# Optimization experiments

Measured on AMD Instinct MI355X. Metric: run time of the kernel, lower is better.

The kernel has to match this reference:

```python
import jax, jax.numpy as jnp
import numpy as np

B, N1, N2, D = 4096, 16, 32, 30   # node batch, 1st-hop nbrs, 2nd-hop nbrs, nodeDataLen
H, HD = 6, 5                       # heads, head_dim (embed_dim = size_out*heads = 30)
LH = 64                            # linear_hidden
NEG_SLOPE = 0.02


def setup_inputs() -> dict:
    key = jax.random.key(0)
    ks = jax.random.split(key, 20)
    def w(k, shape, std=0.2):
        return jax.random.normal(k, shape, dtype=jnp.float32) * std
    return {
        "x2": jax.random.normal(ks[0], (B, N1, N2, D), dtype=jnp.float32),
        "self_feat": jax.random.normal(ks[1], (B, D), dtype=jnp.float32),
        # second-hop GraphLayer params (size_in=30 -> embed 30)
        "lin_w2": w(ks[2], (D, D)), "lin_b2": jnp.zeros((D,), jnp.float32),
        "in_w2": w(ks[3], (3 * D, D), 0.1), "in_b2": jnp.zeros((3 * D,), jnp.float32),
        "out_w2": w(ks[4], (D, D), 0.1), "out_b2": jnp.zeros((D,), jnp.float32),
        # first-hop GraphLayer params
        "lin_w1": w(ks[5], (D, D)), "lin_b1": jnp.zeros((D,), jnp.float32),
        "in_w1": w(ks[6], (3 * D, D), 0.1), "in_b1": jnp.zeros((3 * D,), jnp.float32),
        "out_w1": w(ks[7], (D, D), 0.1), "out_b1": jnp.zeros((D,), jnp.float32),
        # classification MLP
        "cw1": w(ks[8], (LH, D), 0.02), "cb1": jnp.zeros((LH,), jnp.float32),
        "cw2": w(ks[9], (LH, LH), 0.02), "cb2": jnp.zeros((LH,), jnp.float32),
        "cw3": w(ks[10], (2, LH), 0.02), "cb3": jnp.zeros((2,), jnp.float32),
    }


def graph_layer(x, lw, lb, iw, ib, ow, ob):
    """x: [S, D] -> Linear + LeakyReLU(0.02) + MHA(self) + mean over S -> [D].
    Dropout(0.2) is identity in eval mode."""
    S = x.shape[0]
    y = jax.nn.leaky_relu(x @ lw.T + lb, NEG_SLOPE)          # [S, D]
    qkv = y @ iw.T + ib                                       # [S, 3D] packed in_proj
    q, k, v = jnp.split(qkv, 3, axis=-1)
    q = q.reshape(S, H, HD)
    k = k.reshape(S, H, HD)
    v = v.reshape(S, H, HD)
    scores = jnp.einsum('shd,thd->hst', q, k) / np.float32(np.sqrt(HD))
    att = jax.nn.softmax(scores, axis=-1)                     # [H, S, S]
    o = jnp.einsum('hst,thd->shd', att, v).reshape(S, H * HD) # [S, D]
    o = o @ ow.T + ob
    return o.mean(axis=0)                                     # [D]


def reference(x2, self_feat,
              lin_w2, lin_b2, in_w2, in_b2, out_w2, out_b2,
              lin_w1, lin_b1, in_w1, in_b1, out_w1, out_b1,
              cw1, cb1, cw2, cb2, cw3, cb3):
    gl2 = lambda x: graph_layer(x, lin_w2, lin_b2, in_w2, in_b2, out_w2, out_b2)
    h1 = jax.vmap(jax.vmap(gl2))(x2)                          # [B, N1, D] second-hop aggregation
    seq = jnp.concatenate([h1, self_feat[:, None, :]], axis=1)  # [B, N1+1, D] append current node
    gl1 = lambda x: graph_layer(x, lin_w1, lin_b1, in_w1, in_b1, out_w1, out_b1)
    emb = jax.vmap(gl1)(seq)                                  # [B, D]
    h = jax.nn.leaky_relu(emb @ cw1.T + cb1, NEG_SLOPE)
    h = jax.nn.leaky_relu(h @ cw2.T + cb2, NEG_SLOPE)
    logits = h @ cw3.T + cb3                                  # [B, 2]
    # original applies Softmax(dim=0) to the 1-D 2-vector per node == softmax over classes
    return jax.nn.softmax(logits, axis=-1)
```

## Files before the change

kernel.cpp:

```cpp
#include <hip/hip_runtime.h>
#include <math.h>

#define LRELU(v) fmaxf((v), 0.02f * (v))

typedef __attribute__((ext_vector_type(8)))  short short8;
typedef __attribute__((ext_vector_type(4)))  float f32x4;
typedef __attribute__((ext_vector_type(16))) float f32x16;
typedef __attribute__((ext_vector_type(2)))  int   int2v;
typedef __attribute__((ext_vector_type(4)))  int   int4v;

__device__ inline short f2bf(float f) {
    unsigned u = __builtin_bit_cast(unsigned, f);
    unsigned r = (u + 0x7FFFu + ((u >> 16) & 1u)) >> 16;
    return (short)r;
}
__device__ inline int cvt_pk_bf16(float lo, float hi) {
    int r;
    asm("v_cvt_pk_bf16_f32 %0, %1, %2" : "=v"(r) : "v"(lo), "v"(hi));
    return r;
}
__device__ inline float exp2_asm(float x) {
    float r;
    asm("v_exp_f32 %0, %1" : "=v"(r) : "v"(x));
    return r;
}

#define RS5L  0.6451994329f

__global__ __launch_bounds__(256, 4) void fused_kernel(
    const float* __restrict__ x2, const float* __restrict__ self_feat,
    const float* __restrict__ lw2, const float* __restrict__ lb2,
    const float* __restrict__ iw2, const float* __restrict__ ib2,
    const float* __restrict__ ow2, const float* __restrict__ ob2,
    const float* __restrict__ lw1, const float* __restrict__ lb1,
    const float* __restrict__ iw1, const float* __restrict__ ib1,
    const float* __restrict__ ow1, const float* __restrict__ ob1,
    const float* __restrict__ cw1, const float* __restrict__ cb1,
    const float* __restrict__ cw2, const float* __restrict__ cb2,
    const float* __restrict__ cw3, const float* __restrict__ cb3,
    float* __restrict__ out)
{
    __shared__ __attribute__((aligned(16))) short y_lds[2][32][40];
    __shared__ __attribute__((aligned(16))) short qmf[2][6][33][8];
    __shared__ __attribute__((aligned(16))) short kmf[2][6][33][8];
    __shared__ __attribute__((aligned(16))) short vbf[2][6][8][40];
    __shared__ __attribute__((aligned(16))) float h1f[16][33];
    __shared__ float obar[2][32];
    __shared__ float embb[32];
    __shared__ float hb1[64];
    __shared__ float hb2[64];
    __shared__ float lg[2];

    const int tid  = threadIdx.x;
    const int lane = tid & 63;
    const int w    = tid >> 6;
    const int l15  = lane & 15;
    const int lq   = lane >> 4;
    const int h5   = lane >> 5;
    const int scol = lane & 31;
    const int rowz = (lane < 32) ? scol : 32;

    for (int i = tid; i < 1584; i += 256) { ((int*)qmf)[i] = 0; ((int*)kmf)[i] = 0; }
    for (int i = tid; i < 1920; i += 256) ((int*)vbf)[i] = 0;
    if (tid < 4) obar[tid >> 1][30 + (tid & 1)] = 0.0f;

    const int di = w & 1, si = w >> 1;
    const int jtA = (3 * w) >> 1, jtB = (3 * w + 2) >> 1;
    short8 blw2f; float lbv2v;
    {
        int d = di * 16 + l15;
        #pragma unroll
        for (int i = 0; i < 8; ++i) {
            int k = lq * 8 + i;
            blw2f[i] = f2bf((d < 30 && k < 30) ? lw2[d * 30 + k] : 0.0f);
        }
        lbv2v = (d < 30) ? lb2[d] : 0.0f;
    }
    short8 biwA2, biwB2; float ibvA2, ibvB2;
    {
        int jA = jtA * 16 + l15, jB = jtB * 16 + l15;
        #pragma unroll
        for (int i = 0; i < 8; ++i) {
            int k = lq * 8 + i;
            biwA2[i] = f2bf((jA < 90 && k < 30) ? iw2[jA * 30 + k] : 0.0f);
            biwB2[i] = f2bf((jB < 90 && k < 30) ? iw2[jB * 30 + k] : 0.0f);
        }
        ibvA2 = (jA < 90) ? ib2[jA] : 0.0f;
        ibvB2 = (jB < 90) ? ib2[jB] : 0.0f;
    }
    __syncthreads();

    const long node = (long)blockIdx.x;
    const float* xbase = x2 + node * (16L * 960);
    const float* sfp   = self_feat + node * 30;

    for (int it = 0; it < 8; ++it) {

        {
            int s = si * 16 + l15;
            #pragma unroll
            for (int pr = 0; pr < 2; ++pr) {
                const float* xr = xbase + (2 * it + pr) * 960 + s * 30 + lq * 8;
                float xv[8];
                #pragma unroll
                for (int i = 0; i < 8; ++i) {
                    int k = lq * 8 + i;
                    xv[i] = (k < 30) ? xr[i] : 0.0f;
                }
                int4v ai;
                ai.x = cvt_pk_bf16(xv[0], xv[1]);
                ai.y = cvt_pk_bf16(xv[2], xv[3]);
                ai.z = cvt_pk_bf16(xv[4], xv[5]);
                ai.w = cvt_pk_bf16(xv[6], xv[7]);
                short8 af = __builtin_bit_cast(short8, ai);
                f32x4 c = {0.0f, 0.0f, 0.0f, 0.0f};
                c = __builtin_amdgcn_mfma_f32_16x16x32_bf16(af, blw2f, c, 0, 0, 0);
                float y0 = LRELU(c[0] + lbv2v), y1 = LRELU(c[1] + lbv2v);
                float y2 = LRELU(c[2] + lbv2v), y3 = LRELU(c[3] + lbv2v);
                int p01 = cvt_pk_bf16(y0, y1), p23 = cvt_pk_bf16(y2, y3);
                int row = si * 16 + lq * 4, col = di * 16 + l15;
                y_lds[pr][row + 0][col] = (short)p01;
                y_lds[pr][row + 1][col] = (short)(p01 >> 16);
                y_lds[pr][row + 2][col] = (short)p23;
                y_lds[pr][row + 3][col] = (short)(p23 >> 16);
            }
        }
        __syncthreads();

        {
            #pragma unroll
            for (int pr = 0; pr < 2; ++pr) {
                short8 a0 = *(const short8*)&y_lds[pr][l15][lq * 8];
                short8 a1 = *(const short8*)&y_lds[pr][16 + l15][lq * 8];
                #pragma unroll
                for (int t = 0; t < 3; ++t) {
                    int T = 3 * w + t, jt = T >> 1, si_ = T & 1;
                    short8 a = si_ ? a1 : a0;
                    short8 b = (jt == jtA) ? biwA2 : biwB2;
                    float ibv = (jt == jtA) ? ibvA2 : ibvB2;
                    f32x4 c = {0.0f, 0.0f, 0.0f, 0.0f};
                    c = __builtin_amdgcn_mfma_f32_16x16x32_bf16(a, b, c, 0, 0, 0);
                    int j = jt * 16 + l15;
                    int s0 = si_ * 16 + lq * 4;
                    if (j < 30) {
                        int h = j / 5, e = j - 5 * h;
                        int p01 = cvt_pk_bf16(c[0] + ibv, c[1] + ibv);
                        int p23 = cvt_pk_bf16(c[2] + ibv, c[3] + ibv);
                        qmf[pr][h][s0 + 0][e] = (short)p01;
                        qmf[pr][h][s0 + 1][e] = (short)(p01 >> 16);
                        qmf[pr][h][s0 + 2][e] = (short)p23;
                        qmf[pr][h][s0 + 3][e] = (short)(p23 >> 16);
                    } else if (j < 60) {
                        int jj = j - 30; int h = jj / 5, e = jj - 5 * h;
                        float ibl = ibv * RS5L;
                        int p01 = cvt_pk_bf16(fmaf(c[0], RS5L, ibl), fmaf(c[1], RS5L, ibl));
                        int p23 = cvt_pk_bf16(fmaf(c[2], RS5L, ibl), fmaf(c[3], RS5L, ibl));
                        kmf[pr][h][s0 + 0][e] = (short)p01;
                        kmf[pr][h][s0 + 1][e] = (short)(p01 >> 16);
                        kmf[pr][h][s0 + 2][e] = (short)p23;
                        kmf[pr][h][s0 + 3][e] = (short)(p23 >> 16);
                    } else if (j < 90) {
                        int jj = j - 60; int h = jj / 5, e = jj - 5 * h;
                        int k0 = ((s0 >> 1) & 4) | ((s0 << 1) & 8) | (s0 & 16);
                        int2v wv;
                        wv.x = cvt_pk_bf16(c[0] + ibv, c[1] + ibv);
                        wv.y = cvt_pk_bf16(c[2] + ibv, c[3] + ibv);
                        *(int2v*)&vbf[pr][h][e][k0] = wv;
                    }
                }
            }
        }
        __syncthreads();

        {
            const int pr = w >> 1;
            #pragma unroll
            for (int hh = 0; hh < 3; ++hh) {
                const int h = 3 * (w & 1) + hh;
                short8 af = *(const short8*)&kmf[pr][h][rowz][0];
                short8 bf = *(const short8*)&qmf[pr][h][rowz][0];
                f32x16 c;
                #pragma unroll
                for (int r = 0; r < 16; ++r) c[r] = 0.0f;
                c = __builtin_amdgcn_mfma_f32_32x32x16_bf16(af, bf, c, 0, 0, 0);
                float m = c[0];
                #pragma unroll
                for (int r = 1; r < 16; ++r) m = fmaxf(m, c[r]);
                m = fmaxf(m, __shfl_xor(m, 32));
                float Z = 0.0f;
                #pragma unroll
                for (int r = 0; r < 16; ++r) { c[r] = exp2_asm(c[r] - m); Z += c[r]; }
                Z += __shfl_xor(Z, 32);
                float rZ = __builtin_amdgcn_rcpf(Z) * (1.0f / 32.0f);
                int4v a1i, a2i;
                a1i.x = cvt_pk_bf16(c[0] * rZ,  c[1] * rZ);
                a1i.y = cvt_pk_bf16(c[2] * rZ,  c[3] * rZ);
                a1i.z = cvt_pk_bf16(c[4] * rZ,  c[5] * rZ);
                a1i.w = cvt_pk_bf16(c[6] * rZ,  c[7] * rZ);
                a2i.x = cvt_pk_bf16(c[8] * rZ,  c[9] * rZ);
                a2i.y = cvt_pk_bf16(c[10] * rZ, c[11] * rZ);
                a2i.z = cvt_pk_bf16(c[12] * rZ, c[13] * rZ);
                a2i.w = cvt_pk_bf16(c[14] * rZ, c[15] * rZ);
                short8 b1 = *(const short8*)&vbf[pr][h][scol & 7][8 * h5];
                short8 b2 = *(const short8*)&vbf[pr][h][scol & 7][16 + 8 * h5];
                f32x16 P;
                #pragma unroll
                for (int r = 0; r < 16; ++r) P[r] = 0.0f;
                P = __builtin_amdgcn_mfma_f32_32x32x16_bf16(
                        __builtin_bit_cast(short8, a1i), b1, P, 0, 0, 0);
                P = __builtin_amdgcn_mfma_f32_32x32x16_bf16(
                        __builtin_bit_cast(short8, a2i), b2, P, 0, 0, 0);
                float sm = 0.0f;
                #pragma unroll
                for (int r = 0; r < 16; ++r) sm += P[r];
                sm += __shfl_xor(sm, 32);
                if (lane < 5) obar[pr][h * 5 + lane] = sm;
            }
        }
        __syncthreads();

        if (tid < 240) {
            const int d = tid >> 3, jq = tid & 7;
            #pragma unroll
            for (int pr = 0; pr < 2; ++pr) {
                f32x4 ov = *(const f32x4*)&obar[pr][jq * 4];
                float part = 0.0f;
                #pragma unroll
                for (int i = 0; i < 4; ++i) {
                    int j = jq * 4 + i;
                    if (j < 30) part = fmaf(ov[i], ow2[d * 30 + j], part);
                }
                part += __shfl_down(part, 4, 8);
                part += __shfl_down(part, 2, 8);
                part += __shfl_down(part, 1, 8);
                if (jq == 0) h1f[2 * it + pr][d] = part + ob2[d];
            }
        }
    }
    __syncthreads();

    short8 blw1f; float lbv1v;
    {
        int d = di * 16 + l15;
        #pragma unroll
        for (int i = 0; i < 8; ++i) {
            int k = lq * 8 + i;
            blw1f[i] = f2bf((d < 30 && k < 30) ? lw1[d * 30 + k] : 0.0f);
        }
        lbv1v = (d < 30) ? lb1[d] : 0.0f;
    }
    short8 biwA1, biwB1; float ibvA1, ibvB1;
    {
        int jA = jtA * 16 + l15, jB = jtB * 16 + l15;
        #pragma unroll
        for (int i = 0; i < 8; ++i) {
            int k = lq * 8 + i;
            biwA1[i] = f2bf((jA < 90 && k < 30) ? iw1[jA * 30 + k] : 0.0f);
            biwB1[i] = f2bf((jB < 90 && k < 30) ? iw1[jB * 30 + k] : 0.0f);
        }
        ibvA1 = (jA < 90) ? ib1[jA] : 0.0f;
        ibvB1 = (jB < 90) ? ib1[jB] : 0.0f;
    }

    {
        float xv[8];
        if (si == 0) {
            #pragma unroll
            for (int i = 0; i < 8; ++i) {
                int k = lq * 8 + i;
                xv[i] = (k < 30) ? h1f[l15][k] : 0.0f;
            }
        } else {
            #pragma unroll
            for (int i = 0; i < 8; ++i) {
                int k = lq * 8 + i;
                xv[i] = (l15 == 0 && k < 30) ? sfp[k] : 0.0f;
            }
        }
        int4v ai;
        ai.x = cvt_pk_bf16(xv[0], xv[1]);
        ai.y = cvt_pk_bf16(xv[2], xv[3]);
        ai.z = cvt_pk_bf16(xv[4], xv[5]);
        ai.w = cvt_pk_bf16(xv[6], xv[7]);
        short8 af = __builtin_bit_cast(short8, ai);
        f32x4 c = {0.0f, 0.0f, 0.0f, 0.0f};
        c = __builtin_amdgcn_mfma_f32_16x16x32_bf16(af, blw1f, c, 0, 0, 0);
        float y0 = LRELU(c[0] + lbv1v), y1 = LRELU(c[1] + lbv1v);
        float y2 = LRELU(c[2] + lbv1v), y3 = LRELU(c[3] + lbv1v);
        int p01 = cvt_pk_bf16(y0, y1), p23 = cvt_pk_bf16(y2, y3);
        int row = si * 16 + lq * 4, col = di * 16 + l15;
        y_lds[0][row + 0][col] = (short)p01;
        y_lds[0][row + 1][col] = (short)(p01 >> 16);
        y_lds[0][row + 2][col] = (short)p23;
        y_lds[0][row + 3][col] = (short)(p23 >> 16);
    }
    __syncthreads();

    {
        short8 a0 = *(const short8*)&y_lds[0][l15][lq * 8];
        short8 a1 = *(const short8*)&y_lds[0][16 + l15][lq * 8];
        #pragma unroll
        for (int t = 0; t < 3; ++t) {
            int T = 3 * w + t, jt = T >> 1, si_ = T & 1;
            short8 a = si_ ? a1 : a0;
            short8 b = (jt == jtA) ? biwA1 : biwB1;
            float ibv = (jt == jtA) ? ibvA1 : ibvB1;
            f32x4 c = {0.0f, 0.0f, 0.0f, 0.0f};
            c = __builtin_amdgcn_mfma_f32_16x16x32_bf16(a, b, c, 0, 0, 0);
            int j = jt * 16 + l15;
            int s0 = si_ * 16 + lq * 4;
            if (j < 30) {
                int h = j / 5, e = j - 5 * h;
                int p01 = cvt_pk_bf16(c[0] + ibv, c[1] + ibv);
                int p23 = cvt_pk_bf16(c[2] + ibv, c[3] + ibv);
                qmf[0][h][s0 + 0][e] = (short)p01;
                qmf[0][h][s0 + 1][e] = (short)(p01 >> 16);
                qmf[0][h][s0 + 2][e] = (short)p23;
                qmf[0][h][s0 + 3][e] = (short)(p23 >> 16);
            } else if (j < 60) {
                int jj = j - 30; int h = jj / 5, e = jj - 5 * h;
                float ibl = ibv * RS5L;
                int p01 = cvt_pk_bf16(fmaf(c[0], RS5L, ibl), fmaf(c[1], RS5L, ibl));
                int p23 = cvt_pk_bf16(fmaf(c[2], RS5L, ibl), fmaf(c[3], RS5L, ibl));
                kmf[0][h][s0 + 0][e] = (short)p01;
                kmf[0][h][s0 + 1][e] = (short)(p01 >> 16);
                kmf[0][h][s0 + 2][e] = (short)p23;
                kmf[0][h][s0 + 3][e] = (short)(p23 >> 16);
            } else if (j < 90) {
                int jj = j - 60; int h = jj / 5, e = jj - 5 * h;
                int k0 = ((s0 >> 1) & 4) | ((s0 << 1) & 8) | (s0 & 16);
                int2v wv;
                wv.x = cvt_pk_bf16(c[0] + ibv, c[1] + ibv);
                wv.y = cvt_pk_bf16(c[2] + ibv, c[3] + ibv);
                *(int2v*)&vbf[0][h][e][k0] = wv;
            }
        }
    }
    __syncthreads();

    if (w < 3) {
        #pragma unroll
        for (int hh = 0; hh < 2; ++hh) {
            const int h = 2 * w + hh;
            short8 af = *(const short8*)&kmf[0][h][rowz][0];
            short8 bf = *(const short8*)&qmf[0][h][rowz][0];
            f32x16 c;
            #pragma unroll
            for (int r = 0; r < 16; ++r) c[r] = 0.0f;
            c = __builtin_amdgcn_mfma_f32_32x32x16_bf16(af, bf, c, 0, 0, 0);
            #pragma unroll
            for (int r = 0; r < 16; ++r) {
                int tr = (r & 3) + 8 * (r >> 2) + 4 * h5;
                c[r] = (tr < 17) ? c[r] : -1e30f;
            }
            float m = c[0];
            #pragma unroll
            for (int r = 1; r < 16; ++r) m = fmaxf(m, c[r]);
            m = fmaxf(m, __shfl_xor(m, 32));
            float Z = 0.0f;
            #pragma unroll
            for (int r = 0; r < 16; ++r) { c[r] = exp2_asm(c[r] - m); Z += c[r]; }
            Z += __shfl_xor(Z, 32);
            float rZ = __builtin_amdgcn_rcpf(Z) * (1.0f / 17.0f);
            int4v a1i, a2i;
            a1i.x = cvt_pk_bf16(c[0] * rZ,  c[1] * rZ);
            a1i.y = cvt_pk_bf16(c[2] * rZ,  c[3] * rZ);
            a1i.z = cvt_pk_bf16(c[4] * rZ,  c[5] * rZ);
            a1i.w = cvt_pk_bf16(c[6] * rZ,  c[7] * rZ);
            a2i.x = cvt_pk_bf16(c[8] * rZ,  c[9] * rZ);
            a2i.y = cvt_pk_bf16(c[10] * rZ, c[11] * rZ);
            a2i.z = cvt_pk_bf16(c[12] * rZ, c[13] * rZ);
            a2i.w = cvt_pk_bf16(c[14] * rZ, c[15] * rZ);
            short8 b1 = *(const short8*)&vbf[0][h][scol & 7][8 * h5];
            short8 b2 = *(const short8*)&vbf[0][h][scol & 7][16 + 8 * h5];
            f32x16 P;
            #pragma unroll
            for (int r = 0; r < 16; ++r) P[r] = 0.0f;
            P = __builtin_amdgcn_mfma_f32_32x32x16_bf16(
                    __builtin_bit_cast(short8, a1i), b1, P, 0, 0, 0);
            P = __builtin_amdgcn_mfma_f32_32x32x16_bf16(
                    __builtin_bit_cast(short8, a2i), b2, P, 0, 0, 0);
            float sm = 0.0f;
            #pragma unroll
            for (int r = 0; r < 8; ++r) sm += P[r];
            sm += (h5 == 0) ? P[8] : 0.0f;
            sm += __shfl_xor(sm, 32);
            if (lane < 5) obar[0][h * 5 + lane] = sm;
        }
    }
    __syncthreads();

    if (tid < 240) {
        const int d = tid >> 3, jq = tid & 7;
        f32x4 ov = *(const f32x4*)&obar[0][jq * 4];
        float part = 0.0f;
        #pragma unroll
        for (int i = 0; i < 4; ++i) {
            int j = jq * 4 + i;
            if (j < 30) part = fmaf(ov[i], ow1[d * 30 + j], part);
        }
        part += __shfl_down(part, 4, 8);
        part += __shfl_down(part, 2, 8);
        part += __shfl_down(part, 1, 8);
        if (jq == 0) embb[d] = part + ob1[d];
    }
    __syncthreads();

    {
        const int o = tid >> 2, kq = tid & 3;
        float part = 0.0f;
        #pragma unroll
        for (int i = 0; i < 8; ++i) {
            int k = kq * 8 + i;
            if (k < 30) part = fmaf(embb[k], cw1[o * 30 + k], part);
        }
        part += __shfl_down(part, 2, 4);
        part += __shfl_down(part, 1, 4);
        if (kq == 0) hb1[o] = LRELU(part + cb1[o]);
    }
    __syncthreads();
    {
        const int o = tid >> 2, kq = tid & 3;
        float part = 0.0f;
        #pragma unroll
        for (int i = 0; i < 16; ++i) {
            int k = kq * 16 + i;
            part = fmaf(hb1[k], cw2[o * 64 + k], part);
        }
        part += __shfl_down(part, 2, 4);
        part += __shfl_down(part, 1, 4);
        if (kq == 0) hb2[o] = LRELU(part + cb2[o]);
    }
    __syncthreads();
    if (tid < 128) {
        const int c = tid >> 6, k = tid & 63;
        float part = hb2[k] * cw3[c * 64 + k];
        part += __shfl_down(part, 32);
        part += __shfl_down(part, 16);
        part += __shfl_down(part, 8);
        part += __shfl_down(part, 4);
        part += __shfl_down(part, 2);
        part += __shfl_down(part, 1);
        if (k == 0) lg[c] = part + cb3[c];
    }
    __syncthreads();
    if (tid < 2) {
        float m = fmaxf(lg[0], lg[1]);
        float e0 = __expf(lg[0] - m), e1 = __expf(lg[1] - m);
        float pr = ((tid == 0) ? e0 : e1) / (e0 + e1);
        out[node * 2 + tid] = pr;
    }
}

extern "C" void kernel_launch(void* const* d_in, const int* in_sizes, int n_in,
                              void* d_out, int out_size, void* d_ws, size_t ws_size,
                              hipStream_t stream)
{
    const float* x2        = (const float*)d_in[0];
    const float* self_feat = (const float*)d_in[1];
    const float* lin_w2 = (const float*)d_in[2];
    const float* lin_b2 = (const float*)d_in[3];
    const float* in_w2  = (const float*)d_in[4];
    const float* in_b2  = (const float*)d_in[5];
    const float* out_w2 = (const float*)d_in[6];
    const float* out_b2 = (const float*)d_in[7];
    const float* lin_w1 = (const float*)d_in[8];
    const float* lin_b1 = (const float*)d_in[9];
    const float* in_w1  = (const float*)d_in[10];
    const float* in_b1  = (const float*)d_in[11];
    const float* out_w1 = (const float*)d_in[12];
    const float* out_b1 = (const float*)d_in[13];
    const float* cw1 = (const float*)d_in[14];
    const float* cb1 = (const float*)d_in[15];
    const float* cw2 = (const float*)d_in[16];
    const float* cb2 = (const float*)d_in[17];
    const float* cw3 = (const float*)d_in[18];
    const float* cb3 = (const float*)d_in[19];
    float* outp = (float*)d_out;

    fused_kernel<<<4096, 256, 0, stream>>>(
        x2, self_feat,
        lin_w2, lin_b2, in_w2, in_b2, out_w2, out_b2,
        lin_w1, lin_b1, in_w1, in_b1, out_w1, out_b1,
        cw1, cb1, cw2, cb2, cw3, cb3, outp);
}
```

Before: 539.0 us.

## Prefetch next iteration's x2 tiles into registers and raise occupancy hint

Global loads of the next pair of second-hop neighbour tiles are issued before the attention work of the current iteration and held in registers, so load latency overlaps compute. Launch bounds go from 4 to 5 waves per SIMD at the same time. The 16 extra live floats per thread combined with the tighter register budget could cause spills.

New measurement: 569.6 us. +5.7%, slower.

```diff
diff --git a/kernel.cpp b/kernel.cpp
--- a/kernel.cpp
+++ b/kernel.cpp
@@ -27,7 +27,7 @@
 
 #define RS5L  0.6451994329f
 
-__global__ __launch_bounds__(256, 4) void fused_kernel(
+__global__ __launch_bounds__(256, 5) void fused_kernel(
     const float* __restrict__ x2, const float* __restrict__ self_feat,
     const float* __restrict__ lw2, const float* __restrict__ lb2,
     const float* __restrict__ iw2, const float* __restrict__ ib2,
@@ -93,25 +93,31 @@
     const long node = (long)blockIdx.x;
     const float* xbase = x2 + node * (16L * 960);
     const float* sfp   = self_feat + node * 30;
+    const int srow = si * 16 + l15;
+
+    float xcur[16];
+    {
+        #pragma unroll
+        for (int pr = 0; pr < 2; ++pr) {
+            const float* xr = xbase + pr * 960 + srow * 30 + lq * 8;
+            #pragma unroll
+            for (int i = 0; i < 8; ++i) {
+                int k = lq * 8 + i;
+                xcur[pr * 8 + i] = (k < 30) ? xr[i] : 0.0f;
+            }
+        }
+    }
 
     for (int it = 0; it < 8; ++it) {
 
         {
-            int s = si * 16 + l15;
             #pragma unroll
             for (int pr = 0; pr < 2; ++pr) {
-                const float* xr = xbase + (2 * it + pr) * 960 + s * 30 + lq * 8;
-                float xv[8];
-                #pragma unroll
-                for (int i = 0; i < 8; ++i) {
-                    int k = lq * 8 + i;
-                    xv[i] = (k < 30) ? xr[i] : 0.0f;
-                }
                 int4v ai;
-                ai.x = cvt_pk_bf16(xv[0], xv[1]);
-                ai.y = cvt_pk_bf16(xv[2], xv[3]);
-                ai.z = cvt_pk_bf16(xv[4], xv[5]);
-                ai.w = cvt_pk_bf16(xv[6], xv[7]);
+                ai.x = cvt_pk_bf16(xcur[pr * 8 + 0], xcur[pr * 8 + 1]);
+                ai.y = cvt_pk_bf16(xcur[pr * 8 + 2], xcur[pr * 8 + 3]);
+                ai.z = cvt_pk_bf16(xcur[pr * 8 + 4], xcur[pr * 8 + 5]);
+                ai.w = cvt_pk_bf16(xcur[pr * 8 + 6], xcur[pr * 8 + 7]);
                 short8 af = __builtin_bit_cast(short8, ai);
                 f32x4 c = {0.0f, 0.0f, 0.0f, 0.0f};
                 c = __builtin_amdgcn_mfma_f32_16x16x32_bf16(af, blw2f, c, 0, 0, 0);
@@ -123,6 +129,19 @@
                 y_lds[pr][row + 1][col] = (short)(p01 >> 16);
                 y_lds[pr][row + 2][col] = (short)p23;
                 y_lds[pr][row + 3][col] = (short)(p23 >> 16);
+            }
+        }
+        float xnext[16];
+        {
+            const int itn = (it < 7) ? it + 1 : it;
+            #pragma unroll
+            for (int pr = 0; pr < 2; ++pr) {
+                const float* xr = xbase + (2 * itn + pr) * 960 + srow * 30 + lq * 8;
+                #pragma unroll
+                for (int i = 0; i < 8; ++i) {
+                    int k = lq * 8 + i;
+                    xnext[pr * 8 + i] = (k < 30) ? xr[i] : 0.0f;
+                }
             }
         }
         __syncthreads();
@@ -236,6 +255,8 @@
                 if (jq == 0) h1f[2 * it + pr][d] = part + ob2[d];
             }
         }
+        #pragma unroll
+        for (int i = 0; i < 16; ++i) xcur[i] = xnext[i];
     }
     __syncthreads();
 
```

## Fuse second-hop out-projection into attention waves, removing a barrier per iteration

Applied to the files above, without the earlier changes.

Each wave now applies its partial out_proj (its 3 heads' 15 columns) directly via lane shuffles and writes per-group partial results to a new shared buffer, instead of staging head outputs in shared memory and running a separate 240-thread reduction after a barrier. The two group partials and the bias are summed later when the first-hop layer loads its inputs. This removes one __syncthreads and one LDS round trip per iteration. In exchange it adds shuffles and per-lane global weight loads inside the loop.

Measured after the change: 497.6 us. -7.7%, faster.

```diff
diff --git a/kernel.cpp b/kernel.cpp
--- a/kernel.cpp
+++ b/kernel.cpp
@@ -44,8 +44,8 @@
     __shared__ __attribute__((aligned(16))) short qmf[2][6][33][8];
     __shared__ __attribute__((aligned(16))) short kmf[2][6][33][8];
     __shared__ __attribute__((aligned(16))) short vbf[2][6][8][40];
-    __shared__ __attribute__((aligned(16))) float h1f[16][33];
-    __shared__ float obar[2][32];
+    __shared__ __attribute__((aligned(16))) float h1fp[2][16][33];
+    __shared__ float obar1[32];
     __shared__ float embb[32];
     __shared__ float hb1[64];
     __shared__ float hb2[64];
@@ -62,7 +62,7 @@
 
     for (int i = tid; i < 1584; i += 256) { ((int*)qmf)[i] = 0; ((int*)kmf)[i] = 0; }
     for (int i = tid; i < 1920; i += 256) ((int*)vbf)[i] = 0;
-    if (tid < 4) obar[tid >> 1][30 + (tid & 1)] = 0.0f;
+    if (tid < 2) obar1[30 + tid] = 0.0f;
 
     const int di = w & 1, si = w >> 1;
     const int jtA = (3 * w) >> 1, jtB = (3 * w + 2) >> 1;
@@ -93,6 +93,7 @@
     const long node = (long)blockIdx.x;
     const float* xbase = x2 + node * (16L * 960);
     const float* sfp   = self_feat + node * 30;
+    const int dd = (scol < 30) ? scol : 0;
 
     for (int it = 0; it < 8; ++it) {
 
@@ -173,10 +174,12 @@
         __syncthreads();
 
         {
-            const int pr = w >> 1;
+            const int pr  = w >> 1;
+            const int grp = w & 1;
+            float smv0, smv1, smv2;
             #pragma unroll
             for (int hh = 0; hh < 3; ++hh) {
-                const int h = 3 * (w & 1) + hh;
+                const int h = 3 * grp + hh;
                 short8 af = *(const short8*)&kmf[pr][h][rowz][0];
                 short8 bf = *(const short8*)&qmf[pr][h][rowz][0];
                 f32x16 c;
@@ -214,27 +217,19 @@
                 #pragma unroll
                 for (int r = 0; r < 16; ++r) sm += P[r];
                 sm += __shfl_xor(sm, 32);
-                if (lane < 5) obar[pr][h * 5 + lane] = sm;
-            }
-        }
-        __syncthreads();
-
-        if (tid < 240) {
-            const int d = tid >> 3, jq = tid & 7;
-            #pragma unroll
-            for (int pr = 0; pr < 2; ++pr) {
-                f32x4 ov = *(const f32x4*)&obar[pr][jq * 4];
-                float part = 0.0f;
-                #pragma unroll
-                for (int i = 0; i < 4; ++i) {
-                    int j = jq * 4 + i;
-                    if (j < 30) part = fmaf(ov[i], ow2[d * 30 + j], part);
+                if (hh == 0) smv0 = sm; else if (hh == 1) smv1 = sm; else smv2 = sm;
+            }
+            float part = 0.0f;
+            #pragma unroll
+            for (int hh = 0; hh < 3; ++hh) {
+                float smv = (hh == 0) ? smv0 : (hh == 1) ? smv1 : smv2;
+                #pragma unroll
+                for (int e = 0; e < 5; ++e) {
+                    float ov = __shfl(smv, e);
+                    part = fmaf(ov, ow2[dd * 30 + grp * 15 + hh * 5 + e], part);
                 }
-                part += __shfl_down(part, 4, 8);
-                part += __shfl_down(part, 2, 8);
-                part += __shfl_down(part, 1, 8);
-                if (jq == 0) h1f[2 * it + pr][d] = part + ob2[d];
-            }
+            }
+            if (lane < 30) h1fp[grp][2 * it + pr][lane] = part;
         }
     }
     __syncthreads();
@@ -268,7 +263,8 @@
             #pragma unroll
             for (int i = 0; i < 8; ++i) {
                 int k = lq * 8 + i;
-                xv[i] = (k < 30) ? h1f[l15][k] : 0.0f;
+                xv[i] = (k < 30)
+                    ? (h1fp[0][l15][k] + h1fp[1][l15][k] + ob2[k]) : 0.0f;
             }
         } else {
             #pragma unroll
@@ -385,14 +381,14 @@
             for (int r = 0; r < 8; ++r) sm += P[r];
             sm += (h5 == 0) ? P[8] : 0.0f;
             sm += __shfl_xor(sm, 32);
-            if (lane < 5) obar[0][h * 5 + lane] = sm;
+            if (lane < 5) obar1[h * 5 + lane] = sm;
         }
     }
     __syncthreads();
 
     if (tid < 240) {
         const int d = tid >> 3, jq = tid & 7;
-        f32x4 ov = *(const f32x4*)&obar[0][jq * 4];
+        f32x4 ov = *(const f32x4*)&obar1[jq * 4];
         float part = 0.0f;
         #pragma unroll
         for (int i = 0; i < 4; ++i) {
```
